# Optimization experiments

Measured on AMD Instinct MI355X. Metric: run time of the kernel, lower is better.

Reference implementation:

```python
import jax, jax.numpy as jnp
import numpy as np

H, W, NUM_HEADS = 32, 32, 8


def dwconv3x3(x, w, b):
    # x: (B,C,H,W), w: (C,1,3,3) depthwise, b: (C,)
    y = jax.lax.conv_general_dilated(
        x, w, window_strides=(1, 1), padding='SAME',
        dimension_numbers=('NCHW', 'OIHW', 'NCHW'),
        feature_group_count=x.shape[1])
    return y + b[None, :, None, None]


def conv1x1(x, w, b):
    # x: (B,C,H,W), w: (O,C), b: (O,)
    return jnp.einsum('oc,bchw->bohw', w, x) + b[None, :, None, None]


def layernorm(x, w, b, eps=1e-6):
    mu = x.mean(-1, keepdims=True)
    var = ((x - mu) ** 2).mean(-1, keepdims=True)
    return (x - mu) / jnp.sqrt(var + eps) * w + b


def setup_inputs() -> dict:
    key = jax.random.key(0)
    ks = jax.random.split(key, 12)
    B, N, C = 32, H * W, 512
    Ch = 4 * C  # inverted MLP hidden
    s_lin = 0.02
    s_dw = np.sqrt(2.0 / 9.0)   # fan_out init for 3x3 depthwise
    s_pw1 = np.sqrt(2.0 / Ch)
    s_pw2 = np.sqrt(2.0 / C)
    return {
        'x': jax.random.normal(ks[0], (B, N, C), jnp.float32),
        'cpe_w': jax.random.normal(ks[1], (C, 1, 3, 3), jnp.float32) * s_dw,
        'cpe_b': jnp.zeros((C,), jnp.float32),
        'ln1_w': jnp.ones((C,), jnp.float32),
        'ln1_b': jnp.zeros((C,), jnp.float32),
        'qkv_w': jax.random.normal(ks[2], (3 * C, C), jnp.float32) * s_lin,
        'crpe_w': jax.random.normal(ks[3], (C, 1, 3, 3), jnp.float32) * s_dw,
        'crpe_b': jnp.zeros((C,), jnp.float32),
        'ln2_w': jnp.ones((C,), jnp.float32),
        'ln2_b': jnp.zeros((C,), jnp.float32),
        'fc1_w': jax.random.normal(ks[4], (Ch, C), jnp.float32) * s_pw1,
        'fc1_b': jnp.zeros((Ch,), jnp.float32),
        'dw_w': jax.random.normal(ks[5], (Ch, 1, 3, 3), jnp.float32) * s_dw,
        'dw_b': jnp.zeros((Ch,), jnp.float32),
        'fc2_w': jax.random.normal(ks[6], (C, Ch), jnp.float32) * s_pw2,
        'fc2_b': jnp.zeros((C,), jnp.float32),
    }


def reference(x, cpe_w, cpe_b, ln1_w, ln1_b, qkv_w, crpe_w, crpe_b,
              ln2_w, ln2_b, fc1_w, fc1_b, dw_w, dw_b, fc2_w, fc2_b):
    B, N, C = x.shape
    h = NUM_HEADS
    d = C // h
    scale = d ** -0.5

    # --- Convolutional position encoding: x = x + dwconv(x) ---
    img = x.reshape(B, H, W, C).transpose(0, 3, 1, 2)  # B C H W
    img = img + dwconv3x3(img, cpe_w, cpe_b)
    x = img.transpose(0, 2, 3, 1).reshape(B, N, C)

    # --- Factorized attention + conv relative position encoding ---
    cur = layernorm(x, ln1_w, ln1_b)
    qkv = cur @ qkv_w.T                                 # (B,N,3C)
    qkv = qkv.reshape(B, N, 3, h, d).transpose(2, 0, 3, 1, 4)  # (3,B,h,N,d)
    q, k, v = qkv[0], qkv[1], qkv[2]
    k_softmax = jax.nn.softmax(k, axis=2)               # softmax over tokens N
    ktv = jnp.einsum('bhnk,bhnv->bhkv', k_softmax, v)   # (B,h,d,d)
    factor_att = jnp.einsum('bhnk,bhkv->bhnv', q, ktv)  # (B,h,N,d)
    # crpe: depthwise conv on v as image, elementwise-multiplied by q
    v_img = v.transpose(0, 1, 3, 2).reshape(B, h * d, H, W)
    v_img = dwconv3x3(v_img, crpe_w, crpe_b)
    v_conv = v_img.reshape(B, h, d, N).transpose(0, 1, 3, 2)
    crpe = q * v_conv
    attn_out = (scale * factor_att + crpe).transpose(0, 2, 1, 3).reshape(B, N, C)
    x = x + attn_out

    # --- Inverted MLP (conv-based channel mixing) ---
    cur = layernorm(x, ln2_w, ln2_b)
    img = cur.reshape(B, H, W, C).transpose(0, 3, 1, 2)  # B C H W
    hdn = conv1x1(img, fc1_w, fc1_b)
    hdn = jax.nn.gelu(hdn, approximate=False)
    hdn = hdn + dwconv3x3(hdn, dw_w, dw_b)
    out = conv1x1(hdn, fc2_w, fc2_b)
    x = x + out.transpose(0, 2, 3, 1).reshape(B, N, C)
    return x
```

## Files before the change

kernel.cpp:

```cpp
#include <hip/hip_runtime.h>
#include <hip/hip_bf16.h>

using bf16 = __hip_bfloat16;
using s16x4 = __attribute__((ext_vector_type(4))) short;
using s16x8 = __attribute__((ext_vector_type(8))) short;
using f32x4 = __attribute__((ext_vector_type(4))) float;

#define DI __device__ __forceinline__

template <int N> DI void wvm() {
    if constexpr (N == 8) asm volatile("s_waitcnt vmcnt(8)" ::: "memory");
    else if constexpr (N == 4) asm volatile("s_waitcnt vmcnt(4)" ::: "memory");
    else if constexpr (N == 2) asm volatile("s_waitcnt vmcnt(2)" ::: "memory");
    else asm volatile("s_waitcnt vmcnt(0)" ::: "memory");
}

DI float b2f(short s) { union { unsigned u; float f; } z; z.u = ((unsigned)(unsigned short)s) << 16; return z.f; }
DI short f2b(float f) { bf16 t = __float2bfloat16(f); return *(short*)&t; }

DI float gelu_f(float x) {
    const float t = 0.7978845608f * x * (1.f + 0.044715f * x * x);
    const float e = __expf(2.f * t);
    const float th = 1.f - 2.f / (e + 1.f);
    return 0.5f * x * (1.f + th);
}

DI void ld8(const bf16* p, float* f) {
    s16x8 x = *(const s16x8*)(const void*)p;
#pragma unroll
    for (int c = 0; c < 8; c++) f[c] = b2f(x[c]);
}
DI void ld8(const float* p, float* f) {
    float4 a = *(const float4*)p, b = *(const float4*)(p + 4);
    f[0]=a.x; f[1]=a.y; f[2]=a.z; f[3]=a.w; f[4]=b.x; f[5]=b.y; f[6]=b.z; f[7]=b.w;
}

typedef const __attribute__((address_space(1))) void* gp_t;
typedef __attribute__((address_space(3))) void* lp_t;
DI void gload_lds16(const void* g, void* l) {
    __builtin_amdgcn_global_load_lds((gp_t)g, (lp_t)l, 16, 0, 0);
}

__global__ void diag_k(float* out, float v) { out[0] = v; }

__global__ void f2bf_k(const float* __restrict__ in, bf16* __restrict__ out, int n) {
    int i = (blockIdx.x * 256 + threadIdx.x) * 8;
    if (i >= n) return;
    float f[8];
    ld8(in + i, f);
    s16x8 o;
#pragma unroll
    for (int c = 0; c < 8; c++) o[c] = f2b(f[c]);
    *(s16x8*)(void*)(out + i) = o;
}

DI void tap10(const float* r, float w0, float w1, float w2, float* acc) {
#pragma unroll
    for (int i = 0; i < 8; i++)
        acc[i] += w0 * r[i] + w1 * r[i + 1] + w2 * r[i + 2];
}

template <typename TI, typename TO, bool RESID, int CPL>
__global__ __launch_bounds__(256) void conv4_k(
    const TI* in, long rs, long coff,
    const float* __restrict__ w, const float* __restrict__ bias,
    TO* out, long ors, int gshift)
{
    constexpr int CH = 64 * CPL;
    constexpr int ECNT = CH / 8;
    __shared__ float buf[2][CH][33];
    const int t = threadIdx.x;
    const int band = blockIdx.x & 3;
    const int cg = (blockIdx.x >> 2) & ((1 << gshift) - 1);
    const int img = blockIdx.x >> (2 + gshift);
    const int y0 = band * 8;

    const int spx = t >> 3;
    const int sce = (t & 7) * ECNT;
    const TI* gsrc = in + ((long)img << 10) * rs + coff + (long)cg * CH + sce;

    const int c = t & 63;
    const int xb = (t >> 6) * 8;

    float wv9[9][CPL], bw[CPL];
#pragma unroll
    for (int p = 0; p < CPL; p++) {
        const int gch = cg * CH + c * CPL + p;
#pragma unroll
        for (int j = 0; j < 9; j++) wv9[j][p] = w[gch * 9 + j];
        bw[p] = bias[gch];
    }

    auto stage = [&](int row) {
        float f[ECNT];
        ld8(gsrc + (long)(row * 32 + spx) * rs, f);
        if constexpr (ECNT == 16) ld8(gsrc + (long)(row * 32 + spx) * rs + 8, f + 8);
        float* d = &buf[row & 1][0][0];
#pragma unroll
        for (int k = 0; k < ECNT; k++) {
            const int ch = sce + k;
            const int rr = (CPL == 2) ? ((ch & 1) * 64 + (ch >> 1)) : ch;
            d[rr * 33 + spx] = f[k];
        }
    };
    auto slice = [&](int row, float r[CPL][10]) {
#pragma unroll
        for (int p = 0; p < CPL; p++) {
            const float* s = &buf[row & 1][c + p * 64][0];
            r[p][0] = (xb == 0) ? 0.f : s[xb - 1];
#pragma unroll
            for (int i = 0; i < 8; i++) r[p][1 + i] = s[xb + i];
            r[p][9] = (xb + 8 >= 32) ? 0.f : s[xb + 8];
        }
    };
    auto zero = [&](float r[CPL][10]) {
#pragma unroll
        for (int p = 0; p < CPL; p++)
#pragma unroll
            for (int i = 0; i < 10; i++) r[p][i] = 0.f;
    };

    float r0[CPL][10], r1[CPL][10], r2[CPL][10];
    if (y0 > 0) stage(y0 - 1);
    __syncthreads();
    if (y0 > 0) slice(y0 - 1, r0); else zero(r0);
    stage(y0);
    __syncthreads();
    slice(y0, r1);

    for (int y = y0; y < y0 + 8; ++y) {
        const int yn = y + 1;
        if (yn <= 31) stage(yn);
        __syncthreads();
        if (yn <= 31) slice(yn, r2); else zero(r2);
        float acc[CPL][8];
#pragma unroll
        for (int p = 0; p < CPL; p++) {
#pragma unroll
            for (int i = 0; i < 8; i++) acc[p][i] = bw[p];
            tap10(r0[p], wv9[0][p], wv9[1][p], wv9[2][p], acc[p]);
            tap10(r1[p], wv9[3][p], wv9[4][p], wv9[5][p], acc[p]);
            tap10(r2[p], wv9[6][p], wv9[7][p], wv9[8][p], acc[p]);
            if (RESID) {
#pragma unroll
                for (int i = 0; i < 8; i++) acc[p][i] += r1[p][i + 1];
            }
        }
        TO* o = out + ((long)(img * 1024 + y * 32 + xb)) * ors + (long)cg * CH + c * CPL;
#pragma unroll
        for (int i = 0; i < 8; i++) {
            if constexpr (CPL == 2 && sizeof(TO) == 2) {
                const unsigned u = (unsigned)(unsigned short)f2b(acc[0][i]) |
                                   ((unsigned)(unsigned short)f2b(acc[1][i]) << 16);
                *(unsigned*)(void*)(o + (long)i * ors) = u;
            } else {
                o[(long)i * ors] = (TO)acc[0][i];
            }
        }
#pragma unroll
        for (int p = 0; p < CPL; p++)
#pragma unroll
            for (int i = 0; i < 10; i++) { r0[p][i] = r1[p][i]; r1[p][i] = r2[p][i]; }
    }
}

__global__ __launch_bounds__(256) void ln_k(const float* __restrict__ x,
                                            const float* __restrict__ w,
                                            const float* __restrict__ bp,
                                            bf16* __restrict__ out)
{
    const size_t row = blockIdx.x * 4 + (threadIdx.x >> 6);
    const int t = threadIdx.x & 63;
    const float* xr = x + row * 512;
    alignas(16) float v[8];
    *(float4*)&v[0] = *(const float4*)(xr + t * 8);
    *(float4*)&v[4] = *(const float4*)(xr + t * 8 + 4);
    float s = 0.f;
#pragma unroll
    for (int j = 0; j < 8; j++) s += v[j];
#pragma unroll
    for (int mm = 32; mm; mm >>= 1) s += __shfl_xor(s, mm);
    const float mu = s * (1.f / 512.f);
    float q = 0.f;
#pragma unroll
    for (int j = 0; j < 8; j++) { v[j] -= mu; q += v[j] * v[j]; }
#pragma unroll
    for (int mm = 32; mm; mm >>= 1) q += __shfl_xor(q, mm);
    const float rstd = rsqrtf(q * (1.f / 512.f) + 1e-6f);
    alignas(16) float wv[8], bv[8];
    *(float4*)&wv[0] = *(const float4*)(w + t * 8);
    *(float4*)&wv[4] = *(const float4*)(w + t * 8 + 4);
    *(float4*)&bv[0] = *(const float4*)(bp + t * 8);
    *(float4*)&bv[4] = *(const float4*)(bp + t * 8 + 4);
    alignas(16) bf16 o[8];
#pragma unroll
    for (int j = 0; j < 8; j++) o[j] = __float2bfloat16(v[j] * rstd * wv[j] + bv[j]);
    *(uint4*)(out + row * 512 + t * 8) = *(const uint4*)o;
}

template <int EPI, int K, int NY, bool DUAL = false>
__global__ __launch_bounds__(512) void gemm8p_k(
    const bf16* __restrict__ A, const bf16* __restrict__ A2,
    const bf16* __restrict__ Bw, const float* __restrict__ bias,
    const float* resid, bf16* __restrict__ outb, float* outf, int M, int Nn)
{
    constexpr int KT = K / 64;
    constexpr int LDA = DUAL ? K / 2 : K;
    __shared__ __align__(16) char lds[131072];
    char* ldsA = lds;
    char* ldsB = lds + 65536;
    const int t = threadIdx.x;
    const int lane = t & 63;
    const int w = t >> 6;
    const int wr = w >> 2, wc = w & 3;
    const int nwg = 128 * NY;
    const int swz = (blockIdx.x & 7) * (nwg >> 3) + (blockIdx.x >> 3);
    const int m0 = (swz / NY) * 256;
    const int n0 = (swz % NY) * 256;
    const int lr = lane & 15, lg = lane >> 4;

    f32x4 acc[8][4] = {};

    const int srow = lane >> 3;
    const int ssrc = 8 * ((lane & 7) ^ srow);

    auto SA = [&](int b, int kt, int h) {
        const bf16* Ab = A;
        int ktl = kt;
        if constexpr (DUAL) { if (kt >= KT / 2) { Ab = A2; ktl = kt - KT / 2; } }
#pragma unroll
        for (int j = 0; j < 2; j++) {
            const int lrow0 = j * 64 + w * 8;
            const int R0 = j * 128 + h * 64 + (lrow0 & 63);
            gload_lds16(Ab + (size_t)(m0 + R0 + srow) * LDA + ktl * 64 + ssrc,
                        ldsA + ((b * 2 + h) * 128 + lrow0) * 128);
        }
    };
    auto SB = [&](int b, int kt, int h) {
#pragma unroll
        for (int j = 0; j < 2; j++) {
            const int lrow0 = j * 64 + w * 8;
            const int R0 = (lrow0 >> 5) * 64 + h * 32 + (lrow0 & 31);
            gload_lds16(Bw + (size_t)(n0 + R0 + srow) * K + kt * 64 + ssrc,
                        ldsB + ((b * 2 + h) * 128 + lrow0) * 128);
        }
    };
    auto RA = [&](int b, int h, int m, int ks) -> s16x8 {
        return *(const s16x8*)(ldsA + ((b * 2 + h) * 128 + wr * 64 + m * 16 + lr) * 128
                               + (((ks * 4 + lg) ^ (lr & 7)) << 4));
    };
    auto RB = [&](int b, int h, int n, int ks) -> s16x8 {
        return *(const s16x8*)(ldsB + ((b * 2 + h) * 128 + wc * 32 + n * 16 + lr) * 128
                               + (((ks * 4 + lg) ^ (lr & 7)) << 4));
    };
    auto MM = [&](int mb, int nb, s16x8 (&a)[2][4], s16x8 (&b)[2][2]) {
#pragma unroll
        for (int ks = 0; ks < 2; ks++)
#pragma unroll
            for (int m = 0; m < 4; m++)
#pragma unroll
                for (int n = 0; n < 2; n++)
                    acc[mb + m][nb + n] =
                        __builtin_amdgcn_mfma_f32_16x16x32_bf16(a[ks][m], b[ks][n], acc[mb + m][nb + n], 0, 0, 0);
    };

    SA(0, 0, 0); SB(0, 0, 0); SA(0, 0, 1); SB(0, 0, 1);
    SA(1, 1, 0); SB(1, 1, 0);
    wvm<8>();
    __builtin_amdgcn_s_barrier();

    s16x8 aLo[2][4], aHi[2][4], bLo[2][2], bHi[2][2];
    auto TILE = [&](int kt) {
        const int b = kt & 1;
#pragma unroll
        for (int ks = 0; ks < 2; ks++) {
#pragma unroll
            for (int m = 0; m < 4; m++) aLo[ks][m] = RA(b, 0, m, ks);
#pragma unroll
            for (int n = 0; n < 2; n++) bLo[ks][n] = RB(b, 0, n, ks);
        }
        if (kt + 1 < KT) SA(b ^ 1, kt + 1, 1);
        __builtin_amdgcn_s_barrier();
        __builtin_amdgcn_s_setprio(1);
        MM(0, 0, aLo, bLo);
        __builtin_amdgcn_s_setprio(0);
        if (kt + 1 < KT) wvm<8>(); else wvm<2>();
        __builtin_amdgcn_s_barrier();
#pragma unroll
        for (int ks = 0; ks < 2; ks++)
#pragma unroll
            for (int m = 0; m < 4; m++) aHi[ks][m] = RA(b, 1, m, ks);
        if (kt + 1 < KT) SB(b ^ 1, kt + 1, 1);
        __builtin_amdgcn_s_barrier();
        __builtin_amdgcn_s_setprio(1);
        MM(4, 0, aHi, bLo);
        __builtin_amdgcn_s_setprio(0);
        if (kt + 1 < KT) wvm<8>(); else wvm<0>();
        __builtin_amdgcn_s_barrier();
#pragma unroll
        for (int ks = 0; ks < 2; ks++)
#pragma unroll
            for (int n = 0; n < 2; n++) bHi[ks][n] = RB(b, 1, n, ks);
        if (kt + 2 < KT) SA(b, kt + 2, 0);
        __builtin_amdgcn_s_barrier();
        __builtin_amdgcn_s_setprio(1);
        MM(4, 2, aHi, bHi);
        __builtin_amdgcn_s_setprio(0);
        __builtin_amdgcn_s_barrier();
        if (kt + 2 < KT) SB(b, kt + 2, 0);
        __builtin_amdgcn_s_barrier();
        __builtin_amdgcn_s_setprio(1);
        MM(0, 2, aLo, bHi);
        __builtin_amdgcn_s_setprio(0);
        if (kt + 2 < KT) { wvm<8>(); __builtin_amdgcn_s_barrier(); }
        else if (kt + 1 < KT) { wvm<4>(); __builtin_amdgcn_s_barrier(); }
    };

    if constexpr (KT <= 8) {
#pragma unroll
        for (int kt = 0; kt < KT; ++kt) TILE(kt);
    } else {
#pragma unroll 2
        for (int kt = 0; kt < KT; ++kt) TILE(kt);
    }

#pragma unroll
    for (int i = 0; i < 8; i++) {
#pragma unroll
        for (int j = 0; j < 4; j++) {
            const int col = n0 + wc * 64 + j * 16 + lr;
            float bcol = 0.f;
            if constexpr (EPI >= 1) bcol = bias[col];
#pragma unroll
            for (int r = 0; r < 4; r++) {
                const int row = m0 + wr * 128 + i * 16 + lg * 4 + r;
                float v = acc[i][j][r] + bcol;
                const size_t idx = (size_t)row * Nn + col;
                if (EPI == 2) outf[idx] = v + resid[idx];
                else outb[idx] = __float2bfloat16(EPI == 1 ? gelu_f(v) : v);
            }
        }
    }
}

__global__ __launch_bounds__(256) void ktv3_k(const bf16* __restrict__ qkv,
                                              float* __restrict__ ktvp,
                                              float* __restrict__ csp)
{
    __shared__ __align__(16) char P[64 * 128];
    __shared__ __align__(16) char Vt[64 * 128];
    __shared__ float csl[64 * 5];
    const int t = threadIdx.x;
    const int bh = blockIdx.x >> 1, half = blockIdx.x & 1;
    const int b = bh >> 3, hh = bh & 7;
    const int lane = t & 63, w = t >> 6;
    const int lr = lane & 15, lg = lane >> 4;

    const int n_r = t >> 2;
    const int k0 = (t & 3) * 16;
    const bf16* kbase = qkv + (size_t)(b * 1024) * 1536 + 512 + hh * 64 + k0;
    const bf16* vbase = kbase + 512;

    const int kq = t & 63, qq = t >> 6;
    float cacc = 0.f;

    f32x4 acc[4] = {};

    for (int n0 = half * 512; n0 < half * 512 + 512; n0 += 64) {
        const uint4 ka = *(const uint4*)(kbase + (size_t)(n0 + n_r) * 1536);
        const uint4 kb2 = *(const uint4*)(kbase + (size_t)(n0 + n_r) * 1536 + 8);
        const uint4 va = *(const uint4*)(vbase + (size_t)(n0 + n_r) * 1536);
        const uint4 vb2 = *(const uint4*)(vbase + (size_t)(n0 + n_r) * 1536 + 8);
        __syncthreads();
        {
            const short* ke = (const short*)&ka;
            const short* ke2 = (const short*)&kb2;
            const short* ve = (const short*)&va;
            const short* ve2 = (const short*)&vb2;
            const int nslot = ((n_r >> 3) << 4);
            const int nbyte = (n_r & 7) * 2;
#pragma unroll
            for (int j = 0; j < 16; j++) {
                const int row = k0 + j;
                const short kv = j < 8 ? ke[j] : ke2[j - 8];
                const short vv = j < 8 ? ve[j] : ve2[j - 8];
                const int off = row * 128 + (nslot ^ ((row & 7) << 4)) + nbyte;
                *(short*)(P + off) = f2b(__expf(b2f(kv)));
                *(short*)(Vt + off) = vv;
            }
        }
        __syncthreads();
        {
            const char* pr = P + kq * 128;
            const int sw = (kq & 7) << 4;
            s16x8 x0 = *(const s16x8*)(pr + (((qq * 2) << 4) ^ sw));
            s16x8 x1 = *(const s16x8*)(pr + (((qq * 2 + 1) << 4) ^ sw));
#pragma unroll
            for (int j = 0; j < 8; j++) cacc += b2f(x0[j]) + b2f(x1[j]);
        }
#pragma unroll
        for (int ks2 = 0; ks2 < 2; ks2++) {
            s16x8 aF = *(const s16x8*)(Vt + (w * 16 + lr) * 128 + (((ks2 * 4 + lg) ^ (lr & 7)) << 4));
            s16x8 bF[4];
#pragma unroll
            for (int j = 0; j < 4; j++)
                bF[j] = *(const s16x8*)(P + (j * 16 + lr) * 128 + (((ks2 * 4 + lg) ^ (lr & 7)) << 4));
#pragma unroll
            for (int j = 0; j < 4; j++)
                acc[j] = __builtin_amdgcn_mfma_f32_16x16x32_bf16(aF, bF[j], acc[j], 0, 0, 0);
        }
    }
    __syncthreads();
    csl[kq * 5 + qq] = cacc;
    __syncthreads();
    if (t < 64) csp[blockIdx.x * 64 + t] = csl[t * 5] + csl[t * 5 + 1] + csl[t * 5 + 2] + csl[t * 5 + 3];

    float* o = ktvp + (size_t)blockIdx.x * 4096;
#pragma unroll
    for (int j = 0; j < 4; j++) {
        const int col = j * 16 + lr;
#pragma unroll
        for (int r = 0; r < 4; r++) {
            const int vrow = w * 16 + lg * 4 + r;
            o[vrow * 64 + col] = acc[j][r];
        }
    }
}

__global__ __launch_bounds__(256) void ktvred2_k(const float* __restrict__ ktvp,
                                                 const float* __restrict__ csp,
                                                 bf16* __restrict__ ktvT)
{
    const int bh = blockIdx.x;
    const int t = threadIdx.x;
#pragma unroll
    for (int i = 0; i < 16; i++) {
        const int e = t + 256 * i;
        const int col = e & 63;
        const float cs = csp[(bh * 2) * 64 + col] + csp[(bh * 2 + 1) * 64 + col];
        const float val = ktvp[(size_t)(bh * 2) * 4096 + e] + ktvp[(size_t)(bh * 2 + 1) * 4096 + e];
        ktvT[(size_t)bh * 4096 + e] = __float2bfloat16(val * (0.125f / cs));
    }
}

__global__ __launch_bounds__(256) void attnout2_k(
    float* xs, const bf16* __restrict__ qkv,
    const bf16* __restrict__ ktvT, const bf16* __restrict__ vc)
{
    __shared__ __align__(16) char qs[256 * 128];
    __shared__ __align__(16) char ks[64 * 128];
    const int t = threadIdx.x;
    const int bid = blockIdx.x;
    const int b = bid >> 5, hh = (bid >> 2) & 7, nc = bid & 3;
    const int n0 = nc * 256;
    const int lane = t & 63, w = t >> 6;
    const int lr = lane & 15, lg = lane >> 4;

    {
        const int r0 = t >> 3, sl = t & 7;
#pragma unroll
        for (int it = 0; it < 8; it++) {
            const int row = it * 32 + r0;
            const uint4 v = *(const uint4*)(qkv + ((size_t)(b * 1024 + n0 + row)) * 1536 + hh * 64 + sl * 8);
            *(uint4*)(qs + row * 128 + ((sl ^ (row & 7)) << 4)) = v;
        }
#pragma unroll
        for (int it = 0; it < 2; it++) {
            const int u = it * 256 + t;
            const int vr = u >> 3, sl2 = u & 7;
            const uint4 vv = *(const uint4*)(ktvT + (size_t)(b * 8 + hh) * 4096 + vr * 64 + sl2 * 8);
            *(uint4*)(ks + vr * 128 + ((sl2 ^ (vr & 7)) << 4)) = vv;
        }
    }
    __syncthreads();

    f32x4 acc[4][4] = {};
    s16x8 aF[2][4], bF[2][4];
#pragma unroll
    for (int ksi = 0; ksi < 2; ksi++) {
#pragma unroll
        for (int m = 0; m < 4; m++) {
            const int row = w * 64 + m * 16 + lr;
            aF[ksi][m] = *(const s16x8*)(qs + row * 128 + (((ksi * 4 + lg) ^ (lr & 7)) << 4));
        }
#pragma unroll
        for (int j = 0; j < 4; j++) {
            const int vr = j * 16 + lr;
            bF[ksi][j] = *(const s16x8*)(ks + vr * 128 + (((ksi * 4 + lg) ^ (lr & 7)) << 4));
        }
    }
#pragma unroll
    for (int ksi = 0; ksi < 2; ksi++)
#pragma unroll
        for (int m = 0; m < 4; m++)
#pragma unroll
            for (int j = 0; j < 4; j++)
                acc[m][j] = __builtin_amdgcn_mfma_f32_16x16x32_bf16(aF[ksi][m], bF[ksi][j], acc[m][j], 0, 0, 0);

#pragma unroll
    for (int m = 0; m < 4; m++) {
#pragma unroll
        for (int j = 0; j < 4; j++) {
#pragma unroll
            for (int r = 0; r < 4; r++) {
                const int lrow = w * 64 + m * 16 + lg * 4 + r;
                const int col = j * 16 + lr;
                const size_t idx = ((size_t)(b * 1024 + n0 + lrow)) * 512 + hh * 64 + col;
                const short qv = *(const short*)(qs + lrow * 128 + ((((col >> 3) ^ (lrow & 7)) << 4)) + (col & 7) * 2);
                xs[idx] = xs[idx] + acc[m][j][r] + b2f(qv) * __bfloat162float(vc[idx]);
            }
        }
    }
}

static constexpr size_t OFF_WQ   = 0;
static constexpr size_t OFF_W1   = 1572864;
static constexpr size_t OFF_W2   = 3670016;
static constexpr size_t OFF_CUR  = 5767168;
static constexpr size_t OFF_H2B  = 5767168;
static constexpr size_t OFF_QKV  = 72876032;
static constexpr size_t OFF_HG   = 72876032;
static constexpr size_t OFF_VC   = 173539328;
static constexpr size_t OFF_KTVP = 173539328;
static constexpr size_t OFF_CSP  = 181927936;
static constexpr size_t OFF_H2A  = 139984896;
static constexpr size_t OFF_KTV  = 207093760;
static constexpr size_t WS_NEED  = 207618048;

extern "C" void kernel_launch(void* const* d_in, const int* in_sizes, int n_in,
                              void* d_out, int out_size, void* d_ws, size_t ws_size,
                              hipStream_t stream)
{
    const float* x     = (const float*)d_in[0];
    const float* cpe_w = (const float*)d_in[1];
    const float* cpe_b = (const float*)d_in[2];
    const float* ln1_w = (const float*)d_in[3];
    const float* ln1_b = (const float*)d_in[4];
    const float* qkv_w = (const float*)d_in[5];
    const float* crpe_w= (const float*)d_in[6];
    const float* crpe_b= (const float*)d_in[7];
    const float* ln2_w = (const float*)d_in[8];
    const float* ln2_b = (const float*)d_in[9];
    const float* fc1_w = (const float*)d_in[10];
    const float* fc1_b = (const float*)d_in[11];
    const float* dw_w  = (const float*)d_in[12];
    const float* dw_b  = (const float*)d_in[13];
    const float* fc2_w = (const float*)d_in[14];
    const float* fc2_b = (const float*)d_in[15];
    float* spine = (float*)d_out;
    char* ws = (char*)d_ws;

    if (ws_size < WS_NEED) {
        diag_k<<<1, 1, 0, stream>>>(spine, (float)ws_size);
        return;
    }

    bf16*  wq   = (bf16*)(ws + OFF_WQ);
    bf16*  w1   = (bf16*)(ws + OFF_W1);
    bf16*  w2b  = (bf16*)(ws + OFF_W2);
    bf16*  cur  = (bf16*)(ws + OFF_CUR);
    bf16*  qkv  = (bf16*)(ws + OFF_QKV);
    bf16*  vc   = (bf16*)(ws + OFF_VC);
    float* ktvp = (float*)(ws + OFF_KTVP);
    float* csp  = (float*)(ws + OFF_CSP);
    bf16*  ktvT = (bf16*)(ws + OFF_KTV);
    bf16*  hg   = (bf16*)(ws + OFF_HG);
    bf16*  h2a  = (bf16*)(ws + OFF_H2A);
    bf16*  h2b  = (bf16*)(ws + OFF_H2B);

    f2bf_k<<<(1536 * 512 / 8 + 255) / 256, 256, 0, stream>>>(qkv_w, wq, 1536 * 512);
    f2bf_k<<<(2048 * 512 / 8 + 255) / 256, 256, 0, stream>>>(fc1_w, w1, 2048 * 512);
    f2bf_k<<<(2048 * 512 / 8 + 255) / 256, 256, 0, stream>>>(fc2_w, w2b, 512 * 2048);

    conv4_k<float, float, true, 1><<<32 * 8 * 4, 256, 0, stream>>>(x, 512, 0, cpe_w, cpe_b, spine, 512, 3);

    const int M = 32768;
    ln_k<<<M / 4, 256, 0, stream>>>(spine, ln1_w, ln1_b, cur);
    gemm8p_k<0, 512, 6><<<768, 512, 0, stream>>>(cur, nullptr, wq, nullptr, nullptr, qkv, nullptr, M, 1536);
    ktv3_k<<<512, 256, 0, stream>>>(qkv, ktvp, csp);
    ktvred2_k<<<256, 256, 0, stream>>>(ktvp, csp, ktvT);
    conv4_k<bf16, bf16, false, 2><<<32 * 4 * 4, 256, 0, stream>>>(qkv, 1536, 1024, crpe_w, crpe_b, vc, 512, 2);
    attnout2_k<<<32 * 8 * 4, 256, 0, stream>>>(spine, qkv, ktvT, vc);
    ln_k<<<M / 4, 256, 0, stream>>>(spine, ln2_w, ln2_b, cur);

    gemm8p_k<1, 512, 4><<<512, 512, 0, stream>>>(cur, nullptr, w1, fc1_b, nullptr, hg, nullptr, M, 1024);
    conv4_k<bf16, bf16, true, 2><<<32 * 8 * 4, 256, 0, stream>>>(hg, 1024, 0, dw_w, dw_b, h2a, 1024, 3);
    gemm8p_k<1, 512, 4><<<512, 512, 0, stream>>>(cur, nullptr, w1 + (size_t)1024 * 512, fc1_b + 1024, nullptr, hg, nullptr, M, 1024);
    conv4_k<bf16, bf16, true, 2><<<32 * 8 * 4, 256, 0, stream>>>(hg, 1024, 0, dw_w + (size_t)1024 * 9, dw_b + 1024, h2b, 1024, 3);
    gemm8p_k<2, 2048, 2, true><<<256, 512, 0, stream>>>(h2a, h2b, w2b, fc2_b, spine, nullptr, spine, M, 512);
}
```

Baseline: 471.4 us.

## Use dedicated 128x128-tile GEMM kernel for fc2 projection to raise parallelism

After: 466.6 us. About the same (-1.0%).

```diff
diff --git a/kernel.cpp b/kernel.cpp
--- a/kernel.cpp
+++ b/kernel.cpp
@@ -12,6 +12,7 @@
     if constexpr (N == 8) asm volatile("s_waitcnt vmcnt(8)" ::: "memory");
     else if constexpr (N == 4) asm volatile("s_waitcnt vmcnt(4)" ::: "memory");
     else if constexpr (N == 2) asm volatile("s_waitcnt vmcnt(2)" ::: "memory");
+    else if constexpr (N == 1) asm volatile("s_waitcnt vmcnt(1)" ::: "memory");
     else asm volatile("s_waitcnt vmcnt(0)" ::: "memory");
 }
 
@@ -198,14 +199,12 @@
     *(uint4*)(out + row * 512 + t * 8) = *(const uint4*)o;
 }
 
-template <int EPI, int K, int NY, bool DUAL = false>
+template <int EPI, int K, int NY>
 __global__ __launch_bounds__(512) void gemm8p_k(
-    const bf16* __restrict__ A, const bf16* __restrict__ A2,
-    const bf16* __restrict__ Bw, const float* __restrict__ bias,
-    const float* resid, bf16* __restrict__ outb, float* outf, int M, int Nn)
+    const bf16* __restrict__ A, const bf16* __restrict__ Bw,
+    const float* __restrict__ bias, bf16* __restrict__ outb, int M, int Nn)
 {
     constexpr int KT = K / 64;
-    constexpr int LDA = DUAL ? K / 2 : K;
     __shared__ __align__(16) char lds[131072];
     char* ldsA = lds;
     char* ldsB = lds + 65536;
@@ -225,14 +224,11 @@
     const int ssrc = 8 * ((lane & 7) ^ srow);
 
     auto SA = [&](int b, int kt, int h) {
-        const bf16* Ab = A;
-        int ktl = kt;
-        if constexpr (DUAL) { if (kt >= KT / 2) { Ab = A2; ktl = kt - KT / 2; } }
 #pragma unroll
         for (int j = 0; j < 2; j++) {
             const int lrow0 = j * 64 + w * 8;
             const int R0 = j * 128 + h * 64 + (lrow0 & 63);
-            gload_lds16(Ab + (size_t)(m0 + R0 + srow) * LDA + ktl * 64 + ssrc,
+            gload_lds16(A + (size_t)(m0 + R0 + srow) * K + kt * 64 + ssrc,
                         ldsA + ((b * 2 + h) * 128 + lrow0) * 128);
         }
     };
@@ -316,13 +312,8 @@
         else if (kt + 1 < KT) { wvm<4>(); __builtin_amdgcn_s_barrier(); }
     };
 
-    if constexpr (KT <= 8) {
-#pragma unroll
-        for (int kt = 0; kt < KT; ++kt) TILE(kt);
-    } else {
-#pragma unroll 2
-        for (int kt = 0; kt < KT; ++kt) TILE(kt);
-    }
+#pragma unroll
+    for (int kt = 0; kt < KT; ++kt) TILE(kt);
 
 #pragma unroll
     for (int i = 0; i < 8; i++) {
@@ -336,8 +327,126 @@
                 const int row = m0 + wr * 128 + i * 16 + lg * 4 + r;
                 float v = acc[i][j][r] + bcol;
                 const size_t idx = (size_t)row * Nn + col;
-                if (EPI == 2) outf[idx] = v + resid[idx];
-                else outb[idx] = __float2bfloat16(EPI == 1 ? gelu_f(v) : v);
+                outb[idx] = __float2bfloat16(EPI == 1 ? gelu_f(v) : v);
+            }
+        }
+    }
+}
+
+__global__ __launch_bounds__(512) void gemm8ps_k(
+    const bf16* __restrict__ A, const bf16* __restrict__ A2,
+    const bf16* __restrict__ Bw, const float* __restrict__ bias,
+    const float* resid, float* outf, int M, int Nn)
+{
+    constexpr int KT = 32;
+    __shared__ __align__(16) char lds[65536];
+    char* ldsA = lds;
+    char* ldsB = lds + 32768;
+    const int t = threadIdx.x;
+    const int lane = t & 63;
+    const int w = t >> 6;
+    const int wr = w >> 2, wc = w & 3;
+    const int swz = (blockIdx.x & 7) * 128 + (blockIdx.x >> 3);
+    const int m0 = (swz >> 2) * 128;
+    const int n0 = (swz & 3) * 128;
+    const int lr = lane & 15, lg = lane >> 4;
+
+    f32x4 acc[4][2] = {};
+
+    const int srow = lane >> 3;
+    const int ssrc = 8 * ((lane & 7) ^ srow);
+    const int lrow0 = w * 8;
+
+    auto SA = [&](int b, int kt, int h) {
+        const bf16* Ab = (kt < 16) ? A : A2;
+        const int ktl = (kt < 16) ? kt : kt - 16;
+        const int R0 = h * 64 + lrow0;
+        gload_lds16(Ab + (size_t)(m0 + R0 + srow) * 1024 + ktl * 64 + ssrc,
+                    ldsA + ((b * 2 + h) * 64 + lrow0) * 128);
+    };
+    auto SB = [&](int b, int kt, int h) {
+        const int R0 = (lrow0 >> 4) * 32 + h * 16 + (lrow0 & 15);
+        gload_lds16(Bw + (size_t)(n0 + R0 + srow) * 2048 + kt * 64 + ssrc,
+                    ldsB + ((b * 2 + h) * 64 + lrow0) * 128);
+    };
+    auto RA = [&](int b, int h, int m, int ks) -> s16x8 {
+        return *(const s16x8*)(ldsA + ((b * 2 + h) * 64 + wr * 32 + m * 16 + lr) * 128
+                               + (((ks * 4 + lg) ^ (lr & 7)) << 4));
+    };
+    auto RB = [&](int b, int h, int ks) -> s16x8 {
+        return *(const s16x8*)(ldsB + ((b * 2 + h) * 64 + wc * 16 + lr) * 128
+                               + (((ks * 4 + lg) ^ (lr & 7)) << 4));
+    };
+    auto MM = [&](int hm, int hn, s16x8 (&a)[2][2], s16x8 (&bb)[2]) {
+#pragma unroll
+        for (int ks = 0; ks < 2; ks++)
+#pragma unroll
+            for (int m = 0; m < 2; m++)
+                acc[hm * 2 + m][hn] =
+                    __builtin_amdgcn_mfma_f32_16x16x32_bf16(a[ks][m], bb[ks], acc[hm * 2 + m][hn], 0, 0, 0);
+    };
+
+    SA(0, 0, 0); SB(0, 0, 0); SA(0, 0, 1); SB(0, 0, 1);
+    SA(1, 1, 0); SB(1, 1, 0);
+    wvm<4>();
+    __builtin_amdgcn_s_barrier();
+
+    s16x8 aLo[2][2], aHi[2][2], bLo[2], bHi[2];
+#pragma unroll 2
+    for (int kt = 0; kt < KT; ++kt) {
+        const int b = kt & 1;
+#pragma unroll
+        for (int ks = 0; ks < 2; ks++) {
+#pragma unroll
+            for (int m = 0; m < 2; m++) aLo[ks][m] = RA(b, 0, m, ks);
+            bLo[ks] = RB(b, 0, ks);
+        }
+        if (kt + 1 < KT) SA(b ^ 1, kt + 1, 1);
+        __builtin_amdgcn_s_barrier();
+        __builtin_amdgcn_s_setprio(1);
+        MM(0, 0, aLo, bLo);
+        __builtin_amdgcn_s_setprio(0);
+        if (kt + 1 < KT) wvm<4>(); else wvm<1>();
+        __builtin_amdgcn_s_barrier();
+#pragma unroll
+        for (int ks = 0; ks < 2; ks++)
+#pragma unroll
+            for (int m = 0; m < 2; m++) aHi[ks][m] = RA(b, 1, m, ks);
+        if (kt + 1 < KT) SB(b ^ 1, kt + 1, 1);
+        __builtin_amdgcn_s_barrier();
+        __builtin_amdgcn_s_setprio(1);
+        MM(1, 0, aHi, bLo);
+        __builtin_amdgcn_s_setprio(0);
+        if (kt + 1 < KT) wvm<4>(); else wvm<0>();
+        __builtin_amdgcn_s_barrier();
+#pragma unroll
+        for (int ks = 0; ks < 2; ks++) bHi[ks] = RB(b, 1, ks);
+        if (kt + 2 < KT) SA(b, kt + 2, 0);
+        __builtin_amdgcn_s_barrier();
+        __builtin_amdgcn_s_setprio(1);
+        MM(1, 1, aHi, bHi);
+        __builtin_amdgcn_s_setprio(0);
+        __builtin_amdgcn_s_barrier();
+        if (kt + 2 < KT) SB(b, kt + 2, 0);
+        __builtin_amdgcn_s_barrier();
+        __builtin_amdgcn_s_setprio(1);
+        MM(0, 1, aLo, bHi);
+        __builtin_amdgcn_s_setprio(0);
+        if (kt + 2 < KT) { wvm<4>(); __builtin_amdgcn_s_barrier(); }
+        else if (kt + 1 < KT) { wvm<2>(); __builtin_amdgcn_s_barrier(); }
+    }
+
+#pragma unroll
+    for (int mf = 0; mf < 4; mf++) {
+#pragma unroll
+        for (int nf = 0; nf < 2; nf++) {
+            const int col = n0 + wc * 32 + nf * 16 + lr;
+            const float bcol = bias[col];
+#pragma unroll
+            for (int r = 0; r < 4; r++) {
+                const int row = m0 + (mf >> 1) * 64 + wr * 32 + (mf & 1) * 16 + lg * 4 + r;
+                const size_t idx = (size_t)row * Nn + col;
+                outf[idx] = acc[mf][nf][r] + bcol + resid[idx];
             }
         }
     }
@@ -576,16 +685,16 @@
 
     const int M = 32768;
     ln_k<<<M / 4, 256, 0, stream>>>(spine, ln1_w, ln1_b, cur);
-    gemm8p_k<0, 512, 6><<<768, 512, 0, stream>>>(cur, nullptr, wq, nullptr, nullptr, qkv, nullptr, M, 1536);
+    gemm8p_k<0, 512, 6><<<768, 512, 0, stream>>>(cur, wq, nullptr, qkv, M, 1536);
     ktv3_k<<<512, 256, 0, stream>>>(qkv, ktvp, csp);
     ktvred2_k<<<256, 256, 0, stream>>>(ktvp, csp, ktvT);
     conv4_k<bf16, bf16, false, 2><<<32 * 4 * 4, 256, 0, stream>>>(qkv, 1536, 1024, crpe_w, crpe_b, vc, 512, 2);
     attnout2_k<<<32 * 8 * 4, 256, 0, stream>>>(spine, qkv, ktvT, vc);
     ln_k<<<M / 4, 256, 0, stream>>>(spine, ln2_w, ln2_b, cur);
 
-    gemm8p_k<1, 512, 4><<<512, 512, 0, stream>>>(cur, nullptr, w1, fc1_b, nullptr, hg, nullptr, M, 1024);
+    gemm8p_k<1, 512, 4><<<512, 512, 0, stream>>>(cur, w1, fc1_b, hg, M, 1024);
     conv4_k<bf16, bf16, true, 2><<<32 * 8 * 4, 256, 0, stream>>>(hg, 1024, 0, dw_w, dw_b, h2a, 1024, 3);
-    gemm8p_k<1, 512, 4><<<512, 512, 0, stream>>>(cur, nullptr, w1 + (size_t)1024 * 512, fc1_b + 1024, nullptr, hg, nullptr, M, 1024);
+    gemm8p_k<1, 512, 4><<<512, 512, 0, stream>>>(cur, w1 + (size_t)1024 * 512, fc1_b + 1024, hg, M, 1024);
     conv4_k<bf16, bf16, true, 2><<<32 * 8 * 4, 256, 0, stream>>>(hg, 1024, 0, dw_w + (size_t)1024 * 9, dw_b + 1024, h2b, 1024, 3);
-    gemm8p_k<2, 2048, 2, true><<<256, 512, 0, stream>>>(h2a, h2b, w2b, fc2_b, spine, nullptr, spine, M, 512);
-}
+    gemm8ps_k<<<1024, 512, 0, stream>>>(h2a, h2b, w2b, fc2_b, spine, spine, M, 512);
+}
```
